# Optimization experiments

Measured on AMD Instinct MI355X. Metric: run time of the kernel, lower is better.

## Reference

```python
import jax, jax.numpy as jnp
import numpy as np

N_NODES = 50000


def _sage_max(x, src, dst, W_l, b_l, W_r):
    # gather neighbor (source) features, scatter-max to destination nodes
    msgs = x[src]                                   # [E, F]
    agg = jax.ops.segment_max(msgs, dst, num_segments=N_NODES)  # [N, F], -inf for empty
    agg = jnp.where(jnp.isneginf(agg), 0.0, agg)    # PyG fills isolated nodes with 0
    return agg @ W_l + b_l + x @ W_r                # lin_l(aggr) + lin_r(x)


def setup_inputs() -> dict:
    key = jax.random.key(0)
    ks = jax.random.split(key, 9)
    F_IN, H, OUT, E, EL = 128, 256, 32, 800000, 200000
    x = jax.random.normal(ks[0], (N_NODES, F_IN), dtype=jnp.float32)
    edge_index = jax.random.randint(ks[1], (2, E), 0, N_NODES, dtype=jnp.int64)
    edge_label_index = jax.random.randint(ks[2], (2, EL), 0, N_NODES, dtype=jnp.int64)
    s1 = 1.0 / np.sqrt(F_IN)
    s2 = 1.0 / np.sqrt(H)
    W1_l = jax.random.normal(ks[3], (F_IN, H), dtype=jnp.float32) * s1
    b1 = jnp.zeros((H,), dtype=jnp.float32)
    W1_r = jax.random.normal(ks[4], (F_IN, H), dtype=jnp.float32) * s1
    W2_l = jax.random.normal(ks[5], (H, OUT), dtype=jnp.float32) * s2
    b2 = jnp.zeros((OUT,), dtype=jnp.float32)
    W2_r = jax.random.normal(ks[6], (H, OUT), dtype=jnp.float32) * s2
    return {"x": x, "edge_index": edge_index, "edge_label_index": edge_label_index,
            "W1_l": W1_l, "b1": b1, "W1_r": W1_r,
            "W2_l": W2_l, "b2": b2, "W2_r": W2_r}


def reference(x, edge_index, edge_label_index, W1_l, b1, W1_r, W2_l, b2, W2_r):
    src, dst = edge_index[0], edge_index[1]
    # encode (eval mode: dropout is identity)
    h = jax.nn.relu(_sage_max(x, src, dst, W1_l, b1, W1_r))
    z = _sage_max(h, src, dst, W2_l, b2, W2_r)       # [N, 32]
    # decode: dot product between endpoint embeddings
    s = z[edge_label_index[0]]
    d = z[edge_label_index[1]]
    return jnp.sum(s * d, axis=-1)                   # [E_label]
```

## Files before the change

kernel.cpp:

```cpp
#include <hip/hip_runtime.h>
#include <hip/hip_bf16.h>
#include <math.h>

#define N_NODES 50000
#define NBKT 196
#define BSH 8
#define TILE2 4096
#define CAP 64
#define P2CAP 5888
#define SCAN_FLAG 0x40000000

typedef __attribute__((ext_vector_type(8))) short short8;
typedef __attribute__((ext_vector_type(4))) float f32x4;

static __device__ __forceinline__ float b2f(unsigned int u16) {
    union { unsigned int i; float f; } c; c.i = u16 << 16; return c.f;
}
static __device__ __forceinline__ unsigned int fbits(float f) {
    union { float f; unsigned int i; } c; c.f = f; return c.i;
}
static __device__ __forceinline__ unsigned short f2b_rne(float f) {
    unsigned int u = fbits(f);
    u += 0x7fff + ((u >> 16) & 1);
    return (unsigned short)(u >> 16);
}

static __device__ __forceinline__ unsigned char quant8(float v) {
    int q = (int)(v * 15.9375f + 0.5f);
    return (unsigned char)min(q, 255);
}

static __device__ __forceinline__ unsigned char q8x(float v) {
    int q = __float2int_rn(v * 21.333334f) + 128;
    return (unsigned char)min(max(q, 0), 255);
}

static __device__ __forceinline__ short8 dq8(uint2 v8) {
    short8 r;
#pragma unroll
    for (int bi = 0; bi < 4; ++bi)
        r[bi] = (short)f2b_rne((float)((v8.x >> (8 * bi)) & 255u) * 0.0627451f);
#pragma unroll
    for (int bi = 0; bi < 4; ++bi)
        r[4 + bi] = (short)f2b_rne((float)((v8.y >> (8 * bi)) & 255u) * 0.0627451f);
    return r;
}

#define BYTEMAX16(V) do {                                                             \
    m[0]  = max(m[0],  (int)((V).x & 0xFF));                                          \
    m[1]  = max(m[1],  (int)(((V).x >> 8) & 0xFF));                                   \
    m[2]  = max(m[2],  (int)(((V).x >> 16) & 0xFF));                                  \
    m[3]  = max(m[3],  (int)((V).x >> 24));                                           \
    m[4]  = max(m[4],  (int)((V).y & 0xFF));                                          \
    m[5]  = max(m[5],  (int)(((V).y >> 8) & 0xFF));                                   \
    m[6]  = max(m[6],  (int)(((V).y >> 16) & 0xFF));                                  \
    m[7]  = max(m[7],  (int)((V).y >> 24));                                           \
    m[8]  = max(m[8],  (int)((V).z & 0xFF));                                          \
    m[9]  = max(m[9],  (int)(((V).z >> 8) & 0xFF));                                   \
    m[10] = max(m[10], (int)(((V).z >> 16) & 0xFF));                                  \
    m[11] = max(m[11], (int)((V).z >> 24));                                           \
    m[12] = max(m[12], (int)((V).w & 0xFF));                                          \
    m[13] = max(m[13], (int)(((V).w >> 8) & 0xFF));                                   \
    m[14] = max(m[14], (int)(((V).w >> 16) & 0xFF));                                  \
    m[15] = max(m[15], (int)((V).w >> 24));                                           \
} while (0)


__global__ __launch_bounds__(256) void k_prepbin(
        const float* __restrict__ x, unsigned short* __restrict__ xb,
        unsigned char* __restrict__ x8,
        const float* __restrict__ W1l, const float* __restrict__ W1r, unsigned short* __restrict__ wt1,
        const float* __restrict__ W2l, const float* __restrict__ W2r, unsigned short* __restrict__ wt2,
        float* __restrict__ zb,
        const int* __restrict__ src, const int* __restrict__ dst, int E,
        uint2* __restrict__ tmp, int* __restrict__ cnts, int ntile) {
    __shared__ int cnt[256], sstart[256], lcur[256];
    __shared__ uint2 stage[TILE2];
    const int CX = (N_NODES * 128 / 4) / 256;
    const int CW = CX + 320;
    const int CZ = CW + 1563;
    int b = blockIdx.x, t = threadIdx.x;
    if (b < CX) {
        int i = b * 256 + t;
        float4 v = *(const float4*)(x + (size_t)i * 4);
        ushort4 o;
        o.x = f2b_rne(v.x); o.y = f2b_rne(v.y); o.z = f2b_rne(v.z); o.w = f2b_rne(v.w);
        *(ushort4*)(xb + (size_t)i * 4) = o;
        uchar4 c8;
        c8.x = q8x(v.x); c8.y = q8x(v.y); c8.z = q8x(v.z); c8.w = q8x(v.w);
        *(uchar4*)(x8 + (size_t)i * 4) = c8;
    } else if (b < CX + 256) {
        int i = (b - CX) * 256 + t;
        int n = i >> 8, k = i & 255;
        float v = (k < 128) ? W1l[(size_t)k * 256 + n] : W1r[(size_t)(k - 128) * 256 + n];
        wt1[(size_t)n * 256 + k] = f2b_rne(v);
    } else if (b < CW) {
        int i = (b - CX - 256) * 256 + t;
        int n = i >> 9, k = i & 511;
        float v = (k < 256) ? W2l[(size_t)k * 32 + n] : W2r[(size_t)(k - 256) * 32 + n];
        wt2[(size_t)n * 512 + k] = f2b_rne(v);
    } else if (b < CZ) {
        int i = (b - CW) * 256 + t;
        if (i < 400000) ((float4*)zb)[i] = (float4){0.f, 0.f, 0.f, 0.f};
    } else {
        int tb = b - CZ;
        int e0 = tb * TILE2;
        int tilecnt = min(TILE2, E - e0);
        if (tilecnt <= 0) return;
        cnt[t] = 0;
        __syncthreads();
        if (tilecnt == TILE2) {
            for (int i = 4 * t; i < TILE2; i += 1024) {
                int4 d = *(const int4*)(dst + e0 + i);
                atomicAdd(&cnt[d.x >> BSH], 1);
                atomicAdd(&cnt[d.y >> BSH], 1);
                atomicAdd(&cnt[d.z >> BSH], 1);
                atomicAdd(&cnt[d.w >> BSH], 1);
            }
        } else {
            for (int i = t; i < tilecnt; i += 256)
                atomicAdd(&cnt[dst[e0 + i] >> BSH], 1);
        }
        __syncthreads();
        int cv = cnt[t];
        sstart[t] = cv;
        __syncthreads();
        for (int off = 1; off < 256; off <<= 1) {
            int add = (t >= off) ? sstart[t - off] : 0;
            __syncthreads();
            sstart[t] += add;
            __syncthreads();
        }
        int mystart = sstart[t] - cv;
        __syncthreads();
        sstart[t] = mystart;
        lcur[t] = mystart;
        __syncthreads();
        if (tilecnt == TILE2) {
            for (int i = 4 * t; i < TILE2; i += 1024) {
                int4 d = *(const int4*)(dst + e0 + i);
                int4 s = *(const int4*)(src + e0 + i);
                int q0 = atomicAdd(&lcur[d.x >> BSH], 1); stage[q0] = (uint2){(unsigned)s.x, (unsigned)d.x};
                int q1 = atomicAdd(&lcur[d.y >> BSH], 1); stage[q1] = (uint2){(unsigned)s.y, (unsigned)d.y};
                int q2 = atomicAdd(&lcur[d.z >> BSH], 1); stage[q2] = (uint2){(unsigned)s.z, (unsigned)d.z};
                int q3 = atomicAdd(&lcur[d.w >> BSH], 1); stage[q3] = (uint2){(unsigned)s.w, (unsigned)d.w};
            }
        } else {
            for (int i = t; i < tilecnt; i += 256) {
                int d = dst[e0 + i];
                int s = src[e0 + i];
                int q = atomicAdd(&lcur[d >> BSH], 1);
                uint2 p; p.x = (unsigned)s; p.y = (unsigned)d;
                stage[q] = p;
            }
        }
        __syncthreads();
        if (t < NBKT) cnts[(size_t)t * ntile + tb] = cnt[t];
        for (int i = t; i < tilecnt; i += 256) {
            uint2 p = stage[i];
            int bk = (int)(p.y >> BSH);
            tmp[((size_t)bk * ntile + tb) * CAP + (i - sstart[bk])] = p;
        }
    }
}


__global__ __launch_bounds__(256) void k_bin2(const uint2* __restrict__ tmp,
        const int* __restrict__ cnts, int* __restrict__ pub,
        int* __restrict__ rowptr, int* __restrict__ esrc, int N, int E, int ntile) {
    __shared__ int sc[256], toff[260], nodecnt[256], lcur[256];
    __shared__ int stage[P2CAP];
    __shared__ int shsum[4];
    int k = blockIdx.x, t = threadIdx.x;

    int c = (t < ntile) ? cnts[(size_t)k * ntile + t] : 0;
    sc[t] = c;
    __syncthreads();
    for (int off = 1; off < 256; off <<= 1) {
        int add = (t >= off) ? sc[t - off] : 0;
        __syncthreads();
        sc[t] += add;
        __syncthreads();
    }
    if (t < ntile) toff[t] = sc[t] - c;
    if (t == 255) toff[ntile] = sc[255];
    __syncthreads();
    int total = toff[ntile];

    if (t == 255) atomicExch(&pub[k], SCAN_FLAG | total);
    int v = 0;
    if (t < k) {
        int val;
        do { val = atomicOr(&pub[t], 0); } while (!(val & SCAN_FLAG) || (val & 0x80000000));
        v = val & (SCAN_FLAG - 1);
    }
#pragma unroll
    for (int off = 32; off >= 1; off >>= 1) v += __shfl_xor(v, off);
    if ((t & 63) == 0) shsum[t >> 6] = v;
    nodecnt[t] = 0;
    __syncthreads();
    int base = shsum[0] + shsum[1] + shsum[2] + shsum[3];

    for (int i = t; i < total; i += 256) {
        int lo = 0, hi = ntile;
        while (hi - lo > 1) { int mid = (lo + hi) >> 1; if (toff[mid] <= i) lo = mid; else hi = mid; }
        uint2 p = tmp[((size_t)k * ntile + lo) * CAP + (i - toff[lo])];
        atomicAdd(&nodecnt[(int)p.y & 255], 1);
    }
    __syncthreads();

    int nc = nodecnt[t];
    sc[t] = nc;
    __syncthreads();
    for (int off = 1; off < 256; off <<= 1) {
        int add = (t >= off) ? sc[t - off] : 0;
        __syncthreads();
        sc[t] += add;
        __syncthreads();
    }
    int ex = sc[t] - nc;
    int node = (k << BSH) + t;
    if (node < N) rowptr[node] = base + ex;
    if (node == N) rowptr[N] = E;
    lcur[t] = ex;
    __syncthreads();

    if (total <= P2CAP) {
        for (int i = t; i < total; i += 256) {
            int lo = 0, hi = ntile;
            while (hi - lo > 1) { int mid = (lo + hi) >> 1; if (toff[mid] <= i) lo = mid; else hi = mid; }
            uint2 p = tmp[((size_t)k * ntile + lo) * CAP + (i - toff[lo])];
            int q = atomicAdd(&lcur[(int)p.y & 255], 1);
            stage[q] = (int)p.x;
        }
        __syncthreads();
        for (int i = t; i < total; i += 256)
            esrc[base + i] = stage[i];
    } else {
        for (int i = t; i < total; i += 256) {
            int lo = 0, hi = ntile;
            while (hi - lo > 1) { int mid = (lo + hi) >> 1; if (toff[mid] <= i) lo = mid; else hi = mid; }
            uint2 p = tmp[((size_t)k * ntile + lo) * CAP + (i - toff[lo])];
            int q = atomicAdd(&lcur[(int)p.y & 255], 1);
            esrc[base + q] = (int)p.x;
        }
    }
}


__global__ __launch_bounds__(256) void k_seg_max1(const unsigned char* __restrict__ feat8,
        const int* __restrict__ rowptr, const int* __restrict__ esrc,
        unsigned short* __restrict__ out) {
    int w = threadIdx.x >> 6, t = threadIdx.x & 63;
    int n = blockIdx.x * 4 + w;
    int lane8 = t & 7, sub = t >> 3;
    int beg = rowptr[n], end = rowptr[n + 1];
    int m[16];
#pragma unroll
    for (int k = 0; k < 16; ++k) m[k] = 0;
    for (int base = beg; base < end; base += 64) {
        int cnt = min(64, end - base);
        int vidx = (base + t < end) ? __builtin_nontemporal_load(&esrc[base + t]) : 0;
        for (int j = 0; j < cnt; j += 32) {
            int lim = cnt - j;
            if (lim > 16) {
                uint4 v[4];
#pragma unroll
                for (int u = 0; u < 4; ++u) {
                    int e = min(j + 8 * u + sub, cnt - 1);
                    int s = __shfl(vidx, e);
                    v[u] = *(const uint4*)(feat8 + (size_t)s * 128 + lane8 * 16);
                }
#pragma unroll
                for (int u = 0; u < 4; ++u) BYTEMAX16(v[u]);
            } else if (lim > 8) {
                uint4 v[2];
#pragma unroll
                for (int u = 0; u < 2; ++u) {
                    int e = min(j + 8 * u + sub, cnt - 1);
                    int s = __shfl(vidx, e);
                    v[u] = *(const uint4*)(feat8 + (size_t)s * 128 + lane8 * 16);
                }
#pragma unroll
                for (int u = 0; u < 2; ++u) BYTEMAX16(v[u]);
            } else {
                int e = min(j + sub, cnt - 1);
                int s = __shfl(vidx, e);
                uint4 v0 = *(const uint4*)(feat8 + (size_t)s * 128 + lane8 * 16);
                BYTEMAX16(v0);
            }
        }
    }
#pragma unroll
    for (int k = 0; k < 16; ++k) {
        m[k] = max(m[k], __shfl_xor(m[k], 8));
        m[k] = max(m[k], __shfl_xor(m[k], 16));
        m[k] = max(m[k], __shfl_xor(m[k], 32));
    }
    if (sub == 0) {
        unsigned int pk[8];
#pragma unroll
        for (int k = 0; k < 8; ++k) {
            float f0 = (beg == end) ? 0.f : (float)(m[2 * k]     - 128) * 0.046875f;
            float f1 = (beg == end) ? 0.f : (float)(m[2 * k + 1] - 128) * 0.046875f;
            pk[k] = (fbits(f0) >> 16) | (fbits(f1) & 0xffff0000u);
        }
        uint4 a, b;
        a.x = pk[0]; a.y = pk[1]; a.z = pk[2]; a.w = pk[3];
        b.x = pk[4]; b.y = pk[5]; b.z = pk[6]; b.w = pk[7];
        *(uint4*)(out + (size_t)n * 128 + lane8 * 16) = a;
        *(uint4*)(out + (size_t)n * 128 + lane8 * 16 + 8) = b;
    }
}


__global__ __launch_bounds__(256) void k_seg_max2(const unsigned char* __restrict__ feat8,
        const int* __restrict__ rowptr, const int* __restrict__ esrc,
        unsigned char* __restrict__ out8) {
    int w = threadIdx.x >> 6, t = threadIdx.x & 63;
    int n = blockIdx.x * 4 + w;
    int lane16 = t & 15, sub = t >> 4;
    int beg = rowptr[n], end = rowptr[n + 1];
    int m[16];
#pragma unroll
    for (int k = 0; k < 16; ++k) m[k] = 0;
    for (int base = beg; base < end; base += 64) {
        int cnt = min(64, end - base);
        int vidx = (base + t < end) ? __builtin_nontemporal_load(&esrc[base + t]) : 0;
        for (int j = 0; j < cnt; j += 32) {
            int lim = cnt - j;
            if (lim > 16) {
                uint4 v[8];
#pragma unroll
                for (int u = 0; u < 8; ++u) {
                    int e = min(j + 4 * u + sub, cnt - 1);
                    int s = __shfl(vidx, e);
                    v[u] = *(const uint4*)(feat8 + (size_t)s * 256 + lane16 * 16);
                }
#pragma unroll
                for (int u = 0; u < 8; ++u) BYTEMAX16(v[u]);
            } else if (lim > 8) {
                uint4 v[4];
#pragma unroll
                for (int u = 0; u < 4; ++u) {
                    int e = min(j + 4 * u + sub, cnt - 1);
                    int s = __shfl(vidx, e);
                    v[u] = *(const uint4*)(feat8 + (size_t)s * 256 + lane16 * 16);
                }
#pragma unroll
                for (int u = 0; u < 4; ++u) BYTEMAX16(v[u]);
            } else {
                uint4 v[2];
#pragma unroll
                for (int u = 0; u < 2; ++u) {
                    int e = min(j + 4 * u + sub, cnt - 1);
                    int s = __shfl(vidx, e);
                    v[u] = *(const uint4*)(feat8 + (size_t)s * 256 + lane16 * 16);
                }
#pragma unroll
                for (int u = 0; u < 2; ++u) BYTEMAX16(v[u]);
            }
        }
    }
#pragma unroll
    for (int k = 0; k < 16; ++k) {
        m[k] = max(m[k], __shfl_xor(m[k], 16));
        m[k] = max(m[k], __shfl_xor(m[k], 32));
    }
    if (sub == 0) {
        uint4 p;
        p.x = m[0]  | (m[1]  << 8) | (m[2]  << 16) | (m[3]  << 24);
        p.y = m[4]  | (m[5]  << 8) | (m[6]  << 16) | (m[7]  << 24);
        p.z = m[8]  | (m[9]  << 8) | (m[10] << 16) | (m[11] << 24);
        p.w = m[12] | (m[13] << 8) | (m[14] << 16) | (m[15] << 24);
        *(uint4*)(out8 + (size_t)n * 256 + lane16 * 16) = p;
    }
}


#define STAGE(bi, K0) do {                                                            \
    const unsigned short* Ab_ = ((K0) < 128) ? A0 : A1;                               \
    int kab_ = ((K0) & 127) * 2;                                                      \
    int kbb_ = (K0) * 2;                                                              \
    _Pragma("unroll")                                                                 \
    for (int ii = 0; ii < 2; ++ii) {                                                  \
        int c_ = ii * 256 + tid;                                                      \
        int r_ = c_ >> 2, gs_ = (c_ & 3) ^ (r_ & 3);                                  \
        const char* ga_ = (const char*)Ab_ + (size_t)(m0 + r_) * 256 + kab_ + gs_ * 16; \
        __builtin_amdgcn_global_load_lds(                                             \
            (const __attribute__((address_space(1))) void*)ga_,                       \
            (__attribute__((address_space(3))) void*)((char*)(SH + (bi) * 4096) + (ii * 256 + (tid & ~63)) * 16), \
            16, 0, 0);                                                                \
        const char* gb_ = (const char*)WT + (size_t)(n0 + r_) * 512 + kbb_ + gs_ * 16; \
        __builtin_amdgcn_global_load_lds(                                             \
            (const __attribute__((address_space(1))) void*)gb_,                       \
            (__attribute__((address_space(3))) void*)((char*)(SH + 12288 + (bi) * 4096) + (ii * 256 + (tid & ~63)) * 16), \
            16, 0, 0);                                                                \
    }                                                                                 \
} while (0)

#define VMCNT8() asm volatile("s_waitcnt vmcnt(8)" ::: "memory")
#define VMCNT4() asm volatile("s_waitcnt vmcnt(4)" ::: "memory")
#define VMCNT0() asm volatile("s_waitcnt vmcnt(0)" ::: "memory")
#define SBAR() do { __builtin_amdgcn_sched_barrier(0); __builtin_amdgcn_s_barrier(); __builtin_amdgcn_sched_barrier(0); } while (0)

#define COMPUTE(bi) do {                                                              \
    const short* Asb_ = SH + (bi) * 4096;                                             \
    const short* Bsb_ = SH + 12288 + (bi) * 4096;                                     \
    short8 a_[4], b_[4];                                                              \
    _Pragma("unroll")                                                                 \
    for (int i = 0; i < 4; ++i) {                                                     \
        int r_ = wr * 64 + i * 16 + lane16;                                           \
        a_[i] = *(const short8*)((const char*)Asb_ + r_ * 64 + ((q ^ (r_ & 3)) << 4)); \
    }                                                                                 \
    _Pragma("unroll")                                                                 \
    for (int j = 0; j < 4; ++j) {                                                     \
        int c_ = wc * 64 + j * 16 + lane16;                                           \
        b_[j] = *(const short8*)((const char*)Bsb_ + c_ * 64 + ((q ^ (c_ & 3)) << 4)); \
    }                                                                                 \
    _Pragma("unroll")                                                                 \
    for (int i = 0; i < 4; ++i)                                                       \
        _Pragma("unroll")                                                             \
        for (int j = 0; j < 4; ++j)                                                   \
            acc[i][j] = __builtin_amdgcn_mfma_f32_16x16x32_bf16(a_[i], b_[j], acc[i][j], 0, 0, 0); \
} while (0)

__global__ __launch_bounds__(256) void k_lin1_mfma(
        const unsigned short* __restrict__ A0, const unsigned short* __restrict__ A1,
        const unsigned short* __restrict__ WT, const float* __restrict__ bias,
        const unsigned short* __restrict__ WT2, float* __restrict__ zpart,
        unsigned char* __restrict__ H8, int M) {
    __shared__ __align__(16) short SH[24576];
    short* Hs = SH;

    int tid = threadIdx.x;
    int m0 = blockIdx.y * 128, n0 = blockIdx.x * 128;
    int L = tid & 63, wv = tid >> 6;
    int wr = wv >> 1, wc = wv & 1;
    int lane16 = L & 15, q = L >> 4;

    f32x4 acc[4][4];
#pragma unroll
    for (int i = 0; i < 4; ++i)
#pragma unroll
        for (int j = 0; j < 4; ++j) acc[i][j] = (f32x4){0.f, 0.f, 0.f, 0.f};

    STAGE(0, 0);
    STAGE(1, 32);
    STAGE(2, 64);

    VMCNT8(); SBAR(); COMPUTE(0); SBAR(); STAGE(0, 96);
    VMCNT8(); SBAR(); COMPUTE(1); SBAR(); STAGE(1, 128);
    VMCNT8(); SBAR(); COMPUTE(2); SBAR(); STAGE(2, 160);
    VMCNT8(); SBAR(); COMPUTE(0); SBAR(); STAGE(0, 192);
    VMCNT8(); SBAR(); COMPUTE(1); SBAR(); STAGE(1, 224);
    VMCNT8(); SBAR(); COMPUTE(2);
    VMCNT4(); SBAR(); COMPUTE(0);
    VMCNT0(); SBAR(); COMPUTE(1);

    __syncthreads();

#pragma unroll
    for (int i = 0; i < 4; ++i) {
#pragma unroll
        for (int r = 0; r < 4; ++r) {
            int lrow = wr * 64 + i * 16 + q * 4 + r;
            int row = m0 + lrow;
#pragma unroll
            for (int j = 0; j < 4; ++j) {
                int lcol = wc * 64 + j * 16 + lane16;
                int col = n0 + lcol;
                float v = fmaxf(acc[i][j][r] + bias[col], 0.f);
                Hs[lrow * 136 + lcol] = (short)f2b_rne(v);
                if (row < M) H8[(size_t)row * 256 + col] = quant8(v);
            }
        }
    }
    __syncthreads();

    f32x4 acc2[2][2];
#pragma unroll
    for (int i = 0; i < 2; ++i)
#pragma unroll
        for (int j = 0; j < 2; ++j) acc2[i][j] = (f32x4){0.f, 0.f, 0.f, 0.f};
#pragma unroll
    for (int kk = 0; kk < 4; ++kk) {
        short8 a2[2], b2[2];
#pragma unroll
        for (int i = 0; i < 2; ++i)
            a2[i] = *(const short8*)&Hs[(wv * 32 + i * 16 + lane16) * 136 + kk * 32 + q * 8];
#pragma unroll
        for (int j = 0; j < 2; ++j)
            b2[j] = *(const short8*)(WT2 + (size_t)(j * 16 + lane16) * 512 + 256 + n0 + kk * 32 + q * 8);
#pragma unroll
        for (int i = 0; i < 2; ++i)
#pragma unroll
            for (int j = 0; j < 2; ++j)
                acc2[i][j] = __builtin_amdgcn_mfma_f32_16x16x32_bf16(a2[i], b2[j], acc2[i][j], 0, 0, 0);
    }
#pragma unroll
    for (int i = 0; i < 2; ++i) {
#pragma unroll
        for (int r = 0; r < 4; ++r) {
            int row = m0 + wv * 32 + i * 16 + q * 4 + r;
            if (row >= M) continue;
#pragma unroll
            for (int j = 0; j < 2; ++j) {
                int col = j * 16 + lane16;
                atomicAdd(&zpart[(size_t)row * 32 + col], acc2[i][j][r]);
            }
        }
    }
}


#define LD_FRAGS2(RA, BB0, BB1, K0) do {                                              \
    RA = aok0 ? *(const uint2*)(A8 + (size_t)arow0 * 256 + (K0) + q * 8)              \
              : (uint2){0u, 0u};                                                      \
    BB0 = *(const short8*)(WT + (size_t)lane16 * 512 + (K0) + q * 8);                 \
    BB1 = *(const short8*)(WT + (size_t)(16 + lane16) * 512 + (K0) + q * 8);          \
} while (0)

#define DO_MFMA2(RA, BB0, BB1) do {                                                   \
    short8 a_ = dq8(RA);                                                              \
    acc0 = __builtin_amdgcn_mfma_f32_16x16x32_bf16(a_, BB0, acc0, 0, 0, 0);           \
    acc1 = __builtin_amdgcn_mfma_f32_16x16x32_bf16(a_, BB1, acc1, 0, 0, 0);           \
} while (0)

__global__ __launch_bounds__(256) void k_lin2_mfma(
        const unsigned char* __restrict__ A8,
        const unsigned short* __restrict__ WT, const float* __restrict__ bias,
        float* __restrict__ Z, int M) {
    int tid = threadIdx.x;
    int m0 = blockIdx.x * 64;
    int L = tid & 63, wv = tid >> 6;
    int lane16 = L & 15, q = L >> 4;

    f32x4 acc0 = (f32x4){0.f, 0.f, 0.f, 0.f};
    f32x4 acc1 = (f32x4){0.f, 0.f, 0.f, 0.f};

    int arow0 = m0 + wv * 16 + lane16;
    bool aok0 = arow0 < M;

    uint2 xra, yra;
    short8 xb0, xb1, yb0, yb1;
    LD_FRAGS2(xra, xb0, xb1, 0);
    LD_FRAGS2(yra, yb0, yb1, 32);
    DO_MFMA2(xra, xb0, xb1);
    LD_FRAGS2(xra, xb0, xb1, 64);
    DO_MFMA2(yra, yb0, yb1);
    LD_FRAGS2(yra, yb0, yb1, 96);
    DO_MFMA2(xra, xb0, xb1);
    LD_FRAGS2(xra, xb0, xb1, 128);
    DO_MFMA2(yra, yb0, yb1);
    LD_FRAGS2(yra, yb0, yb1, 160);
    DO_MFMA2(xra, xb0, xb1);
    LD_FRAGS2(xra, xb0, xb1, 192);
    DO_MFMA2(yra, yb0, yb1);
    LD_FRAGS2(yra, yb0, yb1, 224);
    DO_MFMA2(xra, xb0, xb1);
    DO_MFMA2(yra, yb0, yb1);

#pragma unroll
    for (int r = 0; r < 4; ++r) {
        int row = m0 + wv * 16 + q * 4 + r;
        if (row >= M) continue;
#pragma unroll
        for (int j = 0; j < 2; ++j) {
            int col = j * 16 + lane16;
            float av = (j == 0) ? acc0[r] : acc1[r];
            float zp = Z[(size_t)row * 32 + col];
            Z[(size_t)row * 32 + col] = av + bias[col] + zp;
        }
    }
}


__global__ void k_decode(const float* __restrict__ z, const int* __restrict__ eli,
                         int EL, float* __restrict__ out) {
    int tid = blockIdx.x * blockDim.x + threadIdx.x;
    int e = tid >> 3, lane = tid & 7;
    if (e >= EL) return;
    int s = eli[e], d = eli[EL + e];
    float4 a = *((const float4*)(z + (size_t)s * 32) + lane);
    float4 b = *((const float4*)(z + (size_t)d * 32) + lane);
    float dot = a.x * b.x + a.y * b.y + a.z * b.z + a.w * b.w;
    dot += __shfl_xor(dot, 1);
    dot += __shfl_xor(dot, 2);
    dot += __shfl_xor(dot, 4);
    if (lane == 0) out[e] = dot;
}


extern "C" void kernel_launch(void* const* d_in, const int* in_sizes, int n_in,
                              void* d_out, int out_size, void* d_ws, size_t ws_size,
                              hipStream_t stream) {
    const float* x   = (const float*)d_in[0];
    const int*   ei  = (const int*)d_in[1];
    const int*   eli = (const int*)d_in[2];
    const float* W1l = (const float*)d_in[3];
    const float* b1  = (const float*)d_in[4];
    const float* W1r = (const float*)d_in[5];
    const float* W2l = (const float*)d_in[6];
    const float* b2  = (const float*)d_in[7];
    const float* W2r = (const float*)d_in[8];
    float* out = (float*)d_out;

    int N  = N_NODES;
    int E  = in_sizes[1] / 2;
    int EL = in_sizes[2] / 2;
    const int* src = ei;
    const int* dst = ei + E;

    char* ws = (char*)d_ws;
    size_t off = 0;
    auto alloc = [&](size_t bytes) -> void* {
        void* p = ws + off;
        off += (bytes + 255) & ~(size_t)255;
        return p;
    };
    unsigned short* xb   = (unsigned short*)alloc((size_t)N * 128 * 2);
    unsigned char*  x8   = (unsigned char*)alloc((size_t)N * 128);
    unsigned short* aggb = (unsigned short*)alloc((size_t)(N + 128) * 256 * 2);
    unsigned char*  h8   = (unsigned char*)alloc((size_t)N * 256);
    float* zbuf          = (float*)alloc((size_t)N * 32 * 4);
    unsigned short* wt1  = (unsigned short*)alloc(256 * 256 * 2);
    unsigned short* wt2  = (unsigned short*)alloc(32 * 512 * 2);
    int* rowptr   = (int*)alloc((size_t)(N + 1) * 4);
    int ntile     = (E + TILE2 - 1) / TILE2;
    int* cnts     = (int*)alloc((size_t)NBKT * ntile * 4);
    int* pub      = (int*)alloc(256 * 4);
    int* esrc     = (int*)alloc((size_t)E * 4);
    uint2* tmpp   = (uint2*)aggb;
    unsigned char* agg8 = (unsigned char*)aggb;

    const int tb = 256;
    const int CZ = 6250 + 320 + 1563;

    k_prepbin<<<CZ + ntile, tb, 0, stream>>>(x, xb, x8, W1l, W1r, wt1, W2l, W2r, wt2, zbuf,
                                             src, dst, E, tmpp, cnts, ntile);
    k_bin2<<<NBKT, tb, 0, stream>>>(tmpp, cnts, pub, rowptr, esrc, N, E, ntile);

    k_seg_max1<<<(N + 3) / 4, tb, 0, stream>>>(x8, rowptr, esrc, aggb);
    dim3 g1(2, (N + 127) / 128);
    k_lin1_mfma<<<g1, tb, 0, stream>>>(aggb, xb, wt1, b1, wt2, zbuf, h8, N);

    k_seg_max2<<<(N + 3) / 4, tb, 0, stream>>>(h8, rowptr, esrc, agg8);
    k_lin2_mfma<<<(N + 63) / 64, tb, 0, stream>>>(agg8, wt2, b2, zbuf, N);

    k_decode<<<(EL * 8 + 255) / 256, tb, 0, stream>>>(zbuf, eli, EL, out);
}
```

Baseline: 243.1 us.

## Stage lin2 tiles through LDS with async loads; drop binary search in bin2

```diff
diff --git a/kernel.cpp b/kernel.cpp
--- a/kernel.cpp
+++ b/kernel.cpp
@@ -172,6 +172,7 @@
     __shared__ int stage[P2CAP];
     __shared__ int shsum[4];
     int k = blockIdx.x, t = threadIdx.x;
+    int grp = t >> 5, lane32 = t & 31;
 
     int c = (t < ntile) ? cnts[(size_t)k * ntile + t] : 0;
     sc[t] = c;
@@ -201,11 +202,12 @@
     __syncthreads();
     int base = shsum[0] + shsum[1] + shsum[2] + shsum[3];
 
-    for (int i = t; i < total; i += 256) {
-        int lo = 0, hi = ntile;
-        while (hi - lo > 1) { int mid = (lo + hi) >> 1; if (toff[mid] <= i) lo = mid; else hi = mid; }
-        uint2 p = tmp[((size_t)k * ntile + lo) * CAP + (i - toff[lo])];
-        atomicAdd(&nodecnt[(int)p.y & 255], 1);
+    for (int tile = grp; tile < ntile; tile += 8) {
+        int tc = toff[tile + 1] - toff[tile];
+        for (int e = lane32; e < tc; e += 32) {
+            uint2 p = tmp[((size_t)k * ntile + tile) * CAP + e];
+            atomicAdd(&nodecnt[(int)p.y & 255], 1);
+        }
     }
     __syncthreads();
 
@@ -226,23 +228,25 @@
     __syncthreads();
 
     if (total <= P2CAP) {
-        for (int i = t; i < total; i += 256) {
-            int lo = 0, hi = ntile;
-            while (hi - lo > 1) { int mid = (lo + hi) >> 1; if (toff[mid] <= i) lo = mid; else hi = mid; }
-            uint2 p = tmp[((size_t)k * ntile + lo) * CAP + (i - toff[lo])];
-            int q = atomicAdd(&lcur[(int)p.y & 255], 1);
-            stage[q] = (int)p.x;
+        for (int tile = grp; tile < ntile; tile += 8) {
+            int tc = toff[tile + 1] - toff[tile];
+            for (int e = lane32; e < tc; e += 32) {
+                uint2 p = tmp[((size_t)k * ntile + tile) * CAP + e];
+                int q = atomicAdd(&lcur[(int)p.y & 255], 1);
+                stage[q] = (int)p.x;
+            }
         }
         __syncthreads();
         for (int i = t; i < total; i += 256)
             esrc[base + i] = stage[i];
     } else {
-        for (int i = t; i < total; i += 256) {
-            int lo = 0, hi = ntile;
-            while (hi - lo > 1) { int mid = (lo + hi) >> 1; if (toff[mid] <= i) lo = mid; else hi = mid; }
-            uint2 p = tmp[((size_t)k * ntile + lo) * CAP + (i - toff[lo])];
-            int q = atomicAdd(&lcur[(int)p.y & 255], 1);
-            esrc[base + q] = (int)p.x;
+        for (int tile = grp; tile < ntile; tile += 8) {
+            int tc = toff[tile + 1] - toff[tile];
+            for (int e = lane32; e < tc; e += 32) {
+                uint2 p = tmp[((size_t)k * ntile + tile) * CAP + e];
+                int q = atomicAdd(&lcur[(int)p.y & 255], 1);
+                esrc[base + q] = (int)p.x;
+            }
         }
     }
 }
@@ -400,7 +404,9 @@
 } while (0)
 
 #define VMCNT8() asm volatile("s_waitcnt vmcnt(8)" ::: "memory")
+#define VMCNT6() asm volatile("s_waitcnt vmcnt(6)" ::: "memory")
 #define VMCNT4() asm volatile("s_waitcnt vmcnt(4)" ::: "memory")
+#define VMCNT3() asm volatile("s_waitcnt vmcnt(3)" ::: "memory")
 #define VMCNT0() asm volatile("s_waitcnt vmcnt(0)" ::: "memory")
 #define SBAR() do { __builtin_amdgcn_sched_barrier(0); __builtin_amdgcn_s_barrier(); __builtin_amdgcn_sched_barrier(0); } while (0)
 
@@ -514,63 +520,88 @@
 }
 
 
-#define LD_FRAGS2(RA, BB0, BB1, K0) do {                                              \
-    RA = aok0 ? *(const uint2*)(A8 + (size_t)arow0 * 256 + (K0) + q * 8)              \
-              : (uint2){0u, 0u};                                                      \
-    BB0 = *(const short8*)(WT + (size_t)lane16 * 512 + (K0) + q * 8);                 \
-    BB1 = *(const short8*)(WT + (size_t)(16 + lane16) * 512 + (K0) + q * 8);          \
+#define STAGE2(bi, T) do {                                                            \
+    _Pragma("unroll")                                                                 \
+    for (int ii = 0; ii < 2; ++ii) {                                                  \
+        int off_ = (ii * 256 + tid) * 16;                                             \
+        int r_ = off_ >> 6, c_ = off_ & 63;                                           \
+        const char* ga_ = (const char*)A8 + (size_t)(m0 + r_) * 256 + (T) * 64 + c_;  \
+        __builtin_amdgcn_global_load_lds(                                             \
+            (const __attribute__((address_space(1))) void*)ga_,                       \
+            (__attribute__((address_space(3))) void*)(SH8 + (bi) * 8192 + (ii * 256 + (tid & ~63)) * 16), \
+            16, 0, 0);                                                                \
+    }                                                                                 \
+    {                                                                                 \
+        int off_ = tid * 16;                                                          \
+        int r_ = off_ >> 7, c_ = off_ & 127;                                          \
+        const char* gb_ = (const char*)WT + (size_t)r_ * 1024 + (T) * 128 + c_;       \
+        __builtin_amdgcn_global_load_lds(                                             \
+            (const __attribute__((address_space(1))) void*)gb_,                       \
+            (__attribute__((address_space(3))) void*)(SH8 + 24576 + (bi) * 4096 + (tid & ~63) * 16), \
+            16, 0, 0);                                                                \
+    }                                                                                 \
 } while (0)
 
-#define DO_MFMA2(RA, BB0, BB1) do {                                                   \
-    short8 a_ = dq8(RA);                                                              \
-    acc0 = __builtin_amdgcn_mfma_f32_16x16x32_bf16(a_, BB0, acc0, 0, 0, 0);           \
-    acc1 = __builtin_amdgcn_mfma_f32_16x16x32_bf16(a_, BB1, acc1, 0, 0, 0);           \
+#define COMPUTE2(bi) do {                                                             \
+    const unsigned char* As_ = (const unsigned char*)SH8 + (bi) * 8192;               \
+    const char* Bs_ = SH8 + 24576 + (bi) * 4096;                                      \
+    _Pragma("unroll")                                                                 \
+    for (int kk = 0; kk < 64; kk += 32) {                                             \
+        short8 a_[2], b_[2];                                                          \
+        _Pragma("unroll")                                                             \
+        for (int i = 0; i < 2; ++i) {                                                 \
+            uint2 va_ = *(const uint2*)(As_ + (wv * 32 + i * 16 + lane16) * 64 + kk + q * 8); \
+            a_[i] = dq8(va_);                                                         \
+        }                                                                             \
+        _Pragma("unroll")                                                             \
+        for (int j = 0; j < 2; ++j)                                                   \
+            b_[j] = *(const short8*)(Bs_ + (j * 16 + lane16) * 128 + (kk + q * 8) * 2); \
+        _Pragma("unroll")                                                             \
+        for (int i = 0; i < 2; ++i)                                                   \
+            _Pragma("unroll")                                                         \
+            for (int j = 0; j < 2; ++j)                                               \
+                acc[i][j] = __builtin_amdgcn_mfma_f32_16x16x32_bf16(a_[i], b_[j], acc[i][j], 0, 0, 0); \
+    }                                                                                 \
 } while (0)
 
 __global__ __launch_bounds__(256) void k_lin2_mfma(
         const unsigned char* __restrict__ A8,
         const unsigned short* __restrict__ WT, const float* __restrict__ bias,
         float* __restrict__ Z, int M) {
+    __shared__ __align__(16) char SH8[36864];
+
     int tid = threadIdx.x;
-    int m0 = blockIdx.x * 64;
+    int m0 = blockIdx.x * 128;
     int L = tid & 63, wv = tid >> 6;
     int lane16 = L & 15, q = L >> 4;
 
-    f32x4 acc0 = (f32x4){0.f, 0.f, 0.f, 0.f};
-    f32x4 acc1 = (f32x4){0.f, 0.f, 0.f, 0.f};
-
-    int arow0 = m0 + wv * 16 + lane16;
-    bool aok0 = arow0 < M;
-
-    uint2 xra, yra;
-    short8 xb0, xb1, yb0, yb1;
-    LD_FRAGS2(xra, xb0, xb1, 0);
-    LD_FRAGS2(yra, yb0, yb1, 32);
-    DO_MFMA2(xra, xb0, xb1);
-    LD_FRAGS2(xra, xb0, xb1, 64);
-    DO_MFMA2(yra, yb0, yb1);
-    LD_FRAGS2(yra, yb0, yb1, 96);
-    DO_MFMA2(xra, xb0, xb1);
-    LD_FRAGS2(xra, xb0, xb1, 128);
-    DO_MFMA2(yra, yb0, yb1);
-    LD_FRAGS2(yra, yb0, yb1, 160);
-    DO_MFMA2(xra, xb0, xb1);
-    LD_FRAGS2(xra, xb0, xb1, 192);
-    DO_MFMA2(yra, yb0, yb1);
-    LD_FRAGS2(yra, yb0, yb1, 224);
-    DO_MFMA2(xra, xb0, xb1);
-    DO_MFMA2(yra, yb0, yb1);
-
-#pragma unroll
-    for (int r = 0; r < 4; ++r) {
-        int row = m0 + wv * 16 + q * 4 + r;
-        if (row >= M) continue;
-#pragma unroll
-        for (int j = 0; j < 2; ++j) {
-            int col = j * 16 + lane16;
-            float av = (j == 0) ? acc0[r] : acc1[r];
-            float zp = Z[(size_t)row * 32 + col];
-            Z[(size_t)row * 32 + col] = av + bias[col] + zp;
+    f32x4 acc[2][2];
+#pragma unroll
+    for (int i = 0; i < 2; ++i)
+#pragma unroll
+        for (int j = 0; j < 2; ++j) acc[i][j] = (f32x4){0.f, 0.f, 0.f, 0.f};
+
+    STAGE2(0, 0);
+    STAGE2(1, 1);
+    STAGE2(2, 2);
+
+    VMCNT6(); SBAR(); COMPUTE2(0); SBAR(); STAGE2(0, 3);
+    VMCNT6(); SBAR(); COMPUTE2(1);
+    VMCNT3(); SBAR(); COMPUTE2(2);
+    VMCNT0(); SBAR(); COMPUTE2(0);
+
+#pragma unroll
+    for (int i = 0; i < 2; ++i) {
+#pragma unroll
+        for (int r = 0; r < 4; ++r) {
+            int row = m0 + wv * 32 + i * 16 + q * 4 + r;
+            if (row >= M) continue;
+#pragma unroll
+            for (int j = 0; j < 2; ++j) {
+                int col = j * 16 + lane16;
+                float zp = Z[(size_t)row * 32 + col];
+                Z[(size_t)row * 32 + col] = acc[i][j][r] + bias[col] + zp;
+            }
         }
     }
 }
@@ -646,7 +677,7 @@
     k_lin1_mfma<<<g1, tb, 0, stream>>>(aggb, xb, wt1, b1, wt2, zbuf, h8, N);
 
     k_seg_max2<<<(N + 3) / 4, tb, 0, stream>>>(h8, rowptr, esrc, agg8);
-    k_lin2_mfma<<<(N + 63) / 64, tb, 0, stream>>>(agg8, wt2, b2, zbuf, N);
+    k_lin2_mfma<<<(N + 127) / 128, tb, 0, stream>>>(agg8, wt2, b2, zbuf, N);
 
     k_decode<<<(EL * 8 + 255) / 256, tb, 0, stream>>>(zbuf, eli, EL, out);
 }
```

New measurement: 225.8 us. 7.1% less time.
